# Performance work log

Measured on AMD Instinct MI355X. Metric: run time of the kernel, lower is better.

The kernel has to match this reference:

```python
import jax, jax.numpy as jnp
import numpy as np
import math

N_HEADS = 8
LN_EPS = 1e-5


def _segment_softmax(att, seg, n):
    # att: [E, H], seg: [E] target-node ids; grouped softmax over edges per target node
    m = jax.ops.segment_max(att, seg, num_segments=n)
    e = jnp.exp(att - m[seg])
    d = jax.ops.segment_sum(e, seg, num_segments=n)
    return e / (d[seg] + 1e-16)


def _layernorm(h, g, b):
    mu = jnp.mean(h, axis=-1, keepdims=True)
    var = jnp.mean((h - mu) ** 2, axis=-1, keepdims=True)
    return (h - mu) * jax.lax.rsqrt(var + LN_EPS) * g + b


def setup_inputs() -> dict:
    key = jax.random.key(0)
    ks = jax.random.split(key, 16)
    T, N, E, Din, Dh = 3, 20000, 100000, 128, 128
    s = 0.02
    x = jax.random.normal(ks[0], (T, N, Din), dtype=jnp.float32)
    edge_index = jax.random.randint(ks[1], (T, 2, E), 0, N, dtype=jnp.int64)
    return {
        "x": x,
        "edge_index": edge_index,
        "Wq": jax.random.normal(ks[2], (Din, Dh), jnp.float32) * s,
        "bq": jnp.zeros((Dh,), jnp.float32),
        "Wk": jax.random.normal(ks[3], (Din, Dh), jnp.float32) * s,
        "bk": jnp.zeros((Dh,), jnp.float32),
        "Wv": jax.random.normal(ks[4], (Din, Dh), jnp.float32) * s,
        "bv": jnp.zeros((Dh,), jnp.float32),
        "ln_g": jnp.ones((Dh,), jnp.float32),
        "ln_b": jnp.zeros((Dh,), jnp.float32),
        "W1": jax.random.normal(ks[5], (Dh, 2 * Dh), jnp.float32) * s,
        "b1": jnp.zeros((2 * Dh,), jnp.float32),
        "W2": jax.random.normal(ks[6], (2 * Dh, Dh), jnp.float32) * s,
        "b2": jnp.zeros((Dh,), jnp.float32),
    }


def reference(x, edge_index, Wq, bq, Wk, bk, Wv, bv, ln_g, ln_b, W1, b1, W2, b2):
    T, N, _ = x.shape
    Dh = Wq.shape[1]
    dk = Dh // N_HEADS
    inv_sqrt_dk = 1.0 / math.sqrt(dk)

    def ffn(h):
        r = _layernorm(h, ln_g, ln_b)
        r = jax.nn.gelu(r @ W1 + b1, approximate=False)
        r = r @ W2 + b2
        return h + r

    xs, cs, ss = [], [], []
    for t_tar in range(T):
        x_tar = x[t_tar]  # [N, Din]
        # collect edges of times 0..t_tar
        tgt = jnp.concatenate([edge_index[t, 1] for t in range(t_tar + 1)])  # [Ec]
        x_tar_e = x_tar[tgt]  # [Ec, Din]
        x_src_e = jnp.concatenate(
            [x[t][edge_index[t, 0]] for t in range(t_tar + 1)], axis=0
        )  # [Ec, Din]

        q = (x_tar_e @ Wq + bq).reshape(-1, N_HEADS, dk)
        k = (x_src_e @ Wk + bk).reshape(-1, N_HEADS, dk)
        v = (x_src_e @ Wv + bv).reshape(-1, N_HEADS, dk)
        att = jnp.sum(q * k, axis=-1) * inv_sqrt_dk  # [Ec, H]

        res_att = _segment_softmax(att, tgt, N)
        spu_att = _segment_softmax(-att, tgt, N)
        res = (v * res_att[..., None]).reshape(-1, Dh)
        spu = (v * spu_att[..., None]).reshape(-1, Dh)
        causal_hat = jax.ops.segment_sum(res, tgt, num_segments=N)
        spurious_hat = jax.ops.segment_sum(spu, tgt, num_segments=N)

        causal = ffn(causal_hat + x_tar)
        spurious = ffn(spurious_hat)
        xs.append(causal + spurious)
        cs.append(causal)
        ss.append(spurious)
    return (jnp.stack(xs), jnp.stack(cs), jnp.stack(ss))
```

## Files before the change

### kernel.cpp

```cpp
#include <hip/hip_runtime.h>
#include <hip/hip_bf16.h>

#define DEV_INLINE __device__ __forceinline__

namespace {

constexpr int T = 3;
constexpr int NN = 20000;
constexpr int NE = 100000;
constexpr int D = 128;
constexpr int D2 = 256;
constexpr int NROW = T * NN;
constexpr size_t OUTSZ = (size_t)T * NN * D;
constexpr int NTILE = T * (NN / 16);

typedef __attribute__((ext_vector_type(8))) short bf16x8;
typedef __attribute__((ext_vector_type(4))) float f32x4;
typedef __attribute__((ext_vector_type(2))) _Float16 h2;
typedef __hip_bfloat16 bf16;

DEV_INLINE unsigned short f2bf(float f) {
  __hip_bfloat16 t = __float2bfloat16(f);
  return *(unsigned short*)&t;
}

__global__ void k_detect(const unsigned int* __restrict__ ei32, int* __restrict__ flag) {
  int nz = 0;
  for (int i = threadIdx.x; i < 4096; i += 256)
    nz |= (ei32[2 * i + 1] != 0u);
  if (__any(nz) && (threadIdx.x & 63) == 0) atomicOr(&flag[0], 1);
}

DEV_INLINE int loadIdx(const void* ei, int is32, long long idx) {
  return is32 ? ((const int*)ei)[idx] : (int)((const long long*)ei)[idx];
}

__global__ void k_count(const void* __restrict__ ei, const int* __restrict__ flag,
                        int* __restrict__ counts) {
  int i = blockIdx.x * blockDim.x + threadIdx.x;
  if (i >= T * NE) return;
  int is32 = flag[0];
  int t = i / NE, e = i - t * NE;
  int tgt = loadIdx(ei, is32, (long long)(t * 2 + 1) * NE + e);
  atomicAdd(&counts[t * NN + tgt], 1);
}

__global__ void k_scan(const int* __restrict__ counts, int* __restrict__ offsets,
                       int* __restrict__ cursor) {
  int t = blockIdx.x;
  const int* c = counts + t * NN;
  int* o = offsets + t * (NN + 1);
  int* cur = cursor + t * NN;
  __shared__ int part[256];
  int tid = threadIdx.x;
  constexpr int CH = (NN + 255) / 256;
  int b = tid * CH;
  int e = min(b + CH, NN);
  int s = 0;
  for (int i = b; i < e; i++) s += c[i];
  part[tid] = s;
  __syncthreads();
  for (int d = 1; d < 256; d <<= 1) {
    int v = (tid >= d) ? part[tid - d] : 0;
    __syncthreads();
    part[tid] += v;
    __syncthreads();
  }
  int run = part[tid] - s;
  for (int i = b; i < e; i++) { o[i] = run; cur[i] = run; run += c[i]; }
  if (tid == 255) o[NN] = part[255];
}

__global__ void k_scatter(const void* __restrict__ ei, const int* __restrict__ flag,
                          int* __restrict__ cursor, int* __restrict__ elist) {
  int i = blockIdx.x * blockDim.x + threadIdx.x;
  if (i >= T * NE) return;
  int is32 = flag[0];
  int t = i / NE, e = i - t * NE;
  int src = loadIdx(ei, is32, (long long)(t * 2 + 0) * NE + e);
  int tgt = loadIdx(ei, is32, (long long)(t * 2 + 1) * NE + e);
  int pos = atomicAdd(&cursor[t * NN + tgt], 1);
  elist[t * NE + pos] = src;
}

__global__ void k_precast(const float* __restrict__ Wq, const float* __restrict__ Wk,
                          const float* __restrict__ Wv, const float* __restrict__ W1,
                          const float* __restrict__ W2, bf16* __restrict__ WqkvT,
                          bf16* __restrict__ W1L, bf16* __restrict__ W2L) {
  int i0 = blockIdx.x * blockDim.x + threadIdx.x;
  int stride = gridDim.x * blockDim.x;
  for (int j = i0; j < 384 * 128; j += stride) {
    int c = j >> 7, k = j & 127;
    float v = c < 128 ? Wq[k * D + c]
                      : (c < 256 ? Wk[k * D + (c - 128)] : Wv[k * D + (c - 256)]);
    WqkvT[c * 128 + k] = __float2bfloat16(v);
  }
  for (int idx = i0; idx < 4 * 256 * 32; idx += stride) {
    int j = idx & 31, c = (idx >> 5) & 255, kk = idx >> 13;
    W1L[idx] = __float2bfloat16(W1[(kk * 32 + j) * D2 + c]);
  }
  for (int idx = i0; idx < 8 * 128 * 32; idx += stride) {
    int j = idx & 31, c = (idx >> 5) & 127, kk = idx >> 12;
    W2L[idx] = __float2bfloat16(W2[(kk * 32 + j) * D + c]);
  }
}

__global__ __launch_bounds__(256) void k_qkv_mfma(
    const float* __restrict__ x, const bf16* __restrict__ WqkvT,
    const float* __restrict__ bq, const float* __restrict__ bk,
    const float* __restrict__ bv,
    _Float16* __restrict__ Qh, uint2* __restrict__ KV) {
  __shared__ char As[64 * 256];
  __shared__ char Bs[384 * 80];
  int row0 = blockIdx.x * 64;
  int tid = threadIdx.x;
  for (int i = tid; i < 64 * 16; i += 256) {
    int rr = i >> 4, kb = i & 15;
    int grow = row0 + rr;
    uint4 v = make_uint4(0, 0, 0, 0);
    if (grow < NROW) {
      float4 lo = *(const float4*)&x[(size_t)grow * D + kb * 8];
      float4 hi = *(const float4*)&x[(size_t)grow * D + kb * 8 + 4];
      v.x = ((unsigned)f2bf(lo.y) << 16) | f2bf(lo.x);
      v.y = ((unsigned)f2bf(lo.w) << 16) | f2bf(lo.z);
      v.z = ((unsigned)f2bf(hi.y) << 16) | f2bf(hi.x);
      v.w = ((unsigned)f2bf(hi.w) << 16) | f2bf(hi.z);
    }
    *(uint4*)(As + rr * 256 + ((kb * 16) ^ ((rr & 7) << 4))) = v;
  }
  int wid = tid >> 6, lane = tid & 63;
  int lr = lane & 15, lg = lane >> 4;
  f32x4 acc[24];
#pragma unroll
  for (int i = 0; i < 24; i++) acc[i] = (f32x4){0.f, 0.f, 0.f, 0.f};
  for (int kk = 0; kk < 4; kk++) {
    __syncthreads();
    for (int i = tid; i < 384 * 4; i += 256) {
      int c = i >> 2, ko = (i & 3) * 8;
      *(uint4*)(Bs + c * 80 + ko * 2) =
          *(const uint4*)&WqkvT[(size_t)c * 128 + kk * 32 + ko];
    }
    __syncthreads();
    int ar = wid * 16 + lr;
    bf16x8 a = *(bf16x8*)(As + ar * 256 + ((kk * 64 + lg * 16) ^ ((ar & 7) << 4)));
#pragma unroll
    for (int nt = 0; nt < 24; nt++) {
      bf16x8 b = *(bf16x8*)(Bs + (nt * 16 + lr) * 80 + lg * 16);
      acc[nt] = __builtin_amdgcn_mfma_f32_16x16x32_bf16(a, b, acc[nt], 0, 0, 0);
    }
  }
#pragma unroll
  for (int nt = 0; nt < 8; nt++) {
    int c = nt * 16 + lr;
    float bb = bq[c];
#pragma unroll
    for (int j = 0; j < 4; j++) {
      int orow = row0 + wid * 16 + lg * 4 + j;
      if (orow < NROW)
        Qh[(size_t)orow * D + c] = (_Float16)((acc[nt][j] + bb) * 0.25f);
    }
  }
#pragma unroll
  for (int nt = 0; nt < 8; nt++) {
    int c = nt * 16 + lr;
    float bbk = bk[c], bbv = bv[c];
#pragma unroll
    for (int j = 0; j < 4; j++) {
      int orow = row0 + wid * 16 + lg * 4 + j;
      unsigned ku =
          (unsigned)__builtin_bit_cast(unsigned short, (_Float16)(acc[nt + 8][j] + bbk));
      unsigned vu =
          (unsigned)__builtin_bit_cast(unsigned short, (_Float16)(acc[nt + 16][j] + bbv));
      unsigned kn = __shfl_xor(ku, 1, 64);
      unsigned vn = __shfl_xor(vu, 1, 64);
      if ((lr & 1) == 0 && orow < NROW)
        KV[(size_t)orow * 64 + (c >> 1)] = make_uint2((kn << 16) | ku, (vn << 16) | vu);
    }
  }
}

DEV_INLINE float waveReduceSum(float v) {
#pragma unroll
  for (int m = 1; m < 64; m <<= 1) v += __shfl_xor(v, m, 64);
  return v;
}

template <bool B0, bool B1, bool B2>
DEV_INLINE void edgeUpdate(h2 q0, h2 q1, h2 q2, unsigned kraw, unsigned vraw,
                           float& dr0, float& ds0, float& arx0, float& ary0,
                           float& asx0, float& asy0, float& dr1, float& ds1,
                           float& arx1, float& ary1, float& asx1, float& asy1,
                           float& dr2, float& ds2, float& arx2, float& ary2,
                           float& asx2, float& asy2) {
  h2 kh = __builtin_bit_cast(h2, kraw);
  h2 vh = __builtin_bit_cast(h2, vraw);
  float vx = (float)vh[0], vy = (float)vh[1];
  float a0 = 0.f, a1 = 0.f, a2 = 0.f;
  if (B0) a0 = __builtin_amdgcn_fdot2(q0, kh, 0.f, false);
  if (B1) a1 = __builtin_amdgcn_fdot2(q1, kh, 0.f, false);
  if (B2) a2 = __builtin_amdgcn_fdot2(q2, kh, 0.f, false);
  if (B0) a0 += __shfl_xor(a0, 1, 64);
  if (B1) a1 += __shfl_xor(a1, 1, 64);
  if (B2) a2 += __shfl_xor(a2, 1, 64);
  if (B0) a0 += __shfl_xor(a0, 2, 64);
  if (B1) a1 += __shfl_xor(a1, 2, 64);
  if (B2) a2 += __shfl_xor(a2, 2, 64);
  if (B0) a0 += __shfl_xor(a0, 4, 64);
  if (B1) a1 += __shfl_xor(a1, 4, 64);
  if (B2) a2 += __shfl_xor(a2, 4, 64);
  if (B0) {
    float e = __expf(a0), f = __expf(-a0);
    dr0 += e; arx0 += e * vx; ary0 += e * vy;
    ds0 += f; asx0 += f * vx; asy0 += f * vy;
  }
  if (B1) {
    float e = __expf(a1), f = __expf(-a1);
    dr1 += e; arx1 += e * vx; ary1 += e * vy;
    ds1 += f; asx1 += f * vx; asy1 += f * vy;
  }
  if (B2) {
    float e = __expf(a2), f = __expf(-a2);
    dr2 += e; arx2 += e * vx; ary2 += e * vy;
    ds2 += f; asx2 += f * vx; asy2 += f * vy;
  }
}

__global__ __launch_bounds__(256) void k_attn(
    const _Float16* __restrict__ Qh, const uint2* __restrict__ KV,
    const float* __restrict__ x, const int* __restrict__ offsets,
    const int* __restrict__ elist, const float* __restrict__ lng,
    const float* __restrict__ lnb, float* __restrict__ h, bf16* __restrict__ rb) {
  int n = blockIdx.x * 4 + (threadIdx.x >> 6);
  int l = threadIdx.x & 63;
  float2 g2 = *(const float2*)&lng[2 * l];
  float2 b2 = *(const float2*)&lnb[2 * l];
  h2 q0 = __builtin_bit_cast(h2, *(const unsigned*)&Qh[((size_t)0 * NN + n) * D + 2 * l]);
  h2 q1 = __builtin_bit_cast(h2, *(const unsigned*)&Qh[((size_t)1 * NN + n) * D + 2 * l]);
  h2 q2 = __builtin_bit_cast(h2, *(const unsigned*)&Qh[((size_t)2 * NN + n) * D + 2 * l]);
  float dr0 = 0.f, ds0 = 0.f, arx0 = 0.f, ary0 = 0.f, asx0 = 0.f, asy0 = 0.f;
  float dr1 = 0.f, ds1 = 0.f, arx1 = 0.f, ary1 = 0.f, asx1 = 0.f, asy1 = 0.f;
  float dr2 = 0.f, ds2 = 0.f, arx2 = 0.f, ary2 = 0.f, asx2 = 0.f, asy2 = 0.f;
#define TSEC(TT, B0, B1, B2)                                                    \
  {                                                                             \
    const int* off = offsets + TT * (NN + 1);                                   \
    int b = off[n], e = off[n + 1];                                             \
    const int* el = elist + TT * NE;                                            \
    const uint2* KVt = KV + (size_t)TT * NN * 64;                               \
    for (int i = b; i < e; i++) {                                               \
      uint2 kv = KVt[(size_t)el[i] * 64 + l];                                   \
      edgeUpdate<B0, B1, B2>(q0, q1, q2, kv.x, kv.y, dr0, ds0, arx0, ary0,      \
                             asx0, asy0, dr1, ds1, arx1, ary1, asx1, asy1,      \
                             dr2, ds2, arx2, ary2, asx2, asy2);                 \
    }                                                                           \
  }
  TSEC(0, true, true, true)
  TSEC(1, false, true, true)
  TSEC(2, false, false, true)
#undef TSEC
#define EPILOGUE(TT, DR, DS, ARX, ARY, ASX, ASY)                                 \
  {                                                                              \
    float2 xr = *(const float2*)&x[((size_t)TT * NN + n) * D + 2 * l];           \
    float ir = 1.f / (DR + 1e-16f), is = 1.f / (DS + 1e-16f);                    \
    float hcx = ARX * ir + xr.x, hcy = ARY * ir + xr.y;                          \
    float hsx = ASX * is, hsy = ASY * is;                                        \
    float mu = waveReduceSum(hcx + hcy) * (1.f / 128.f);                         \
    float dx = hcx - mu, dy = hcy - mu;                                          \
    float var = waveReduceSum(dx * dx + dy * dy) * (1.f / 128.f);                \
    float rstd = rsqrtf(var + 1e-5f);                                            \
    float rcx = dx * rstd * g2.x + b2.x, rcy = dy * rstd * g2.y + b2.y;          \
    float mu2 = waveReduceSum(hsx + hsy) * (1.f / 128.f);                        \
    float ex = hsx - mu2, ey = hsy - mu2;                                        \
    float var2 = waveReduceSum(ex * ex + ey * ey) * (1.f / 128.f);               \
    float rstd2 = rsqrtf(var2 + 1e-5f);                                          \
    float rsx = ex * rstd2 * g2.x + b2.x, rsy = ey * rstd2 * g2.y + b2.y;        \
    size_t base = (size_t)TT * 2 * NN;                                           \
    size_t iC = (base + n) * D + 2 * l;                                          \
    size_t iS = (base + NN + n) * D + 2 * l;                                     \
    *(float2*)&h[iC] = make_float2(hcx, hcy);                                    \
    *(float2*)&h[iS] = make_float2(hsx, hsy);                                    \
    *(unsigned*)&rb[iC] = ((unsigned)f2bf(rcy) << 16) | f2bf(rcx);               \
    *(unsigned*)&rb[iS] = ((unsigned)f2bf(rsy) << 16) | f2bf(rsx);               \
  }
  EPILOGUE(0, dr0, ds0, arx0, ary0, asx0, asy0)
  EPILOGUE(1, dr1, ds1, arx1, ary1, asx1, asy1)
  EPILOGUE(2, dr2, ds2, arx2, ary2, asx2, asy2)
#undef EPILOGUE
}

__global__ __launch_bounds__(512) void k_ffn_fused(
    const bf16* __restrict__ rb, const bf16* __restrict__ W1L,
    const bf16* __restrict__ W2L, const float* __restrict__ b1,
    const float* __restrict__ b2, const float* __restrict__ h,
    float* __restrict__ out) {
  __shared__ char As[32 * 256];
  __shared__ char Gs[32 * 528];
  int tid = threadIdx.x;
  int wid = tid >> 6, lane = tid & 63;
  int lr = lane & 15, lg = lane >> 4;
  int wr = (wid & 1) * 16;
  int wc1 = (wid >> 1) * 64;
  int wc2 = (wid >> 1) * 32;
  int ar = wr + lr;
  bf16x8 w1f[4][4];
#pragma unroll
  for (int kk = 0; kk < 4; kk++)
#pragma unroll
    for (int nt = 0; nt < 4; nt++)
      w1f[kk][nt] =
          *(const bf16x8*)&W1L[((size_t)kk * 256 + wc1 + nt * 16 + lr) * 32 + lg * 8];
  bf16x8 w2f[8][2];
#pragma unroll
  for (int kk = 0; kk < 8; kk++)
#pragma unroll
    for (int nt = 0; nt < 2; nt++)
      w2f[kk][nt] =
          *(const bf16x8*)&W2L[((size_t)kk * 128 + wc2 + nt * 16 + lr) * 32 + lg * 8];
  float bb1[4], bb2[2];
#pragma unroll
  for (int nt = 0; nt < 4; nt++) bb1[nt] = b1[wc1 + nt * 16 + lr];
#pragma unroll
  for (int nt = 0; nt < 2; nt++) bb2[nt] = b2[wc2 + nt * 16 + lr];
  int srr = tid >> 4, skb = tid & 15;
  int tile = blockIdx.x;
  uint4 pref;
  {
    int t2 = tile / 1250, nb = tile - t2 * 1250;
    size_t grow = (size_t)t2 * 2 * NN + (size_t)(srr >> 4) * NN + nb * 16 + (srr & 15);
    pref = *(const uint4*)&rb[grow * D + skb * 8];
  }
  for (; tile < NTILE; tile += gridDim.x) {
    int t2 = tile / 1250, nb = tile - t2 * 1250;
    int n0 = nb * 16;
    size_t base = (size_t)t2 * 2 * NN;
    *(uint4*)(As + srr * 256 + ((skb * 16) ^ ((srr & 7) << 4))) = pref;
    float hpref[2][4];
#pragma unroll
    for (int nt = 0; nt < 2; nt++) {
      int c = wc2 + nt * 16 + lr;
#pragma unroll
      for (int j = 0; j < 4; j++) {
        int rr2 = wr + lg * 4 + j;
        hpref[nt][j] = h[(base + (size_t)(rr2 >> 4) * NN + n0 + (rr2 & 15)) * D + c];
      }
    }
    int ntile = tile + gridDim.x;
    if (ntile < NTILE) {
      int t2n = ntile / 1250, nbn = ntile - t2n * 1250;
      size_t grow =
          (size_t)t2n * 2 * NN + (size_t)(srr >> 4) * NN + nbn * 16 + (srr & 15);
      pref = *(const uint4*)&rb[grow * D + skb * 8];
    }
    __syncthreads();
    f32x4 acc1[4];
#pragma unroll
    for (int i = 0; i < 4; i++) acc1[i] = (f32x4){0.f, 0.f, 0.f, 0.f};
#pragma unroll
    for (int kk = 0; kk < 4; kk++) {
      bf16x8 a = *(bf16x8*)(As + ar * 256 + ((kk * 64 + lg * 16) ^ ((ar & 7) << 4)));
#pragma unroll
      for (int nt = 0; nt < 4; nt++)
        acc1[nt] =
            __builtin_amdgcn_mfma_f32_16x16x32_bf16(a, w1f[kk][nt], acc1[nt], 0, 0, 0);
    }
#pragma unroll
    for (int nt = 0; nt < 4; nt++) {
      int c = wc1 + nt * 16 + lr;
#pragma unroll
      for (int j = 0; j < 4; j++) {
        int r = wr + lg * 4 + j;
        float y = acc1[nt][j] + bb1[nt];
        y = 0.5f * y * (1.f + erff(y * 0.70710678118654752f));
        unsigned us = f2bf(y);
        unsigned nbv = __shfl_xor(us, 1, 64);
        if ((lr & 1) == 0) *(unsigned*)(Gs + r * 528 + c * 2) = (nbv << 16) | us;
      }
    }
    __syncthreads();
    f32x4 acc2[2];
#pragma unroll
    for (int i = 0; i < 2; i++) acc2[i] = (f32x4){0.f, 0.f, 0.f, 0.f};
#pragma unroll
    for (int kk = 0; kk < 8; kk++) {
      bf16x8 a = *(bf16x8*)(Gs + ar * 528 + kk * 64 + lg * 16);
#pragma unroll
      for (int nt = 0; nt < 2; nt++)
        acc2[nt] =
            __builtin_amdgcn_mfma_f32_16x16x32_bf16(a, w2f[kk][nt], acc2[nt], 0, 0, 0);
    }
    __syncthreads();
    float* zbuf = (float*)Gs;
#pragma unroll
    for (int nt = 0; nt < 2; nt++) {
      int c = wc2 + nt * 16 + lr;
#pragma unroll
      for (int j = 0; j < 4; j++) {
        int rr2 = wr + lg * 4 + j;
        int side = rr2 >> 4;
        int node = n0 + (rr2 & 15);
        float z = acc2[nt][j] + bb2[nt] + hpref[nt][j];
        out[(size_t)(1 + side) * OUTSZ + ((size_t)t2 * NN + node) * D + c] = z;
        zbuf[rr2 * 132 + c] = z;
      }
    }
    __syncthreads();
    for (int i = tid; i < 16 * 128; i += 512) {
      int node = i >> 7, c = i & 127;
      out[((size_t)t2 * NN + n0 + node) * D + c] =
          zbuf[node * 132 + c] + zbuf[(node + 16) * 132 + c];
    }
  }
}

}

extern "C" void kernel_launch(void* const* d_in, const int* in_sizes, int n_in,
                              void* d_out, int out_size, void* d_ws, size_t ws_size,
                              hipStream_t stream) {
  const float* x = (const float*)d_in[0];
  const void* ei = d_in[1];
  const float* Wq = (const float*)d_in[2];
  const float* bq = (const float*)d_in[3];
  const float* Wk = (const float*)d_in[4];
  const float* bk = (const float*)d_in[5];
  const float* Wv = (const float*)d_in[6];
  const float* bv = (const float*)d_in[7];
  const float* lng = (const float*)d_in[8];
  const float* lnb = (const float*)d_in[9];
  const float* W1 = (const float*)d_in[10];
  const float* b1 = (const float*)d_in[11];
  const float* W2 = (const float*)d_in[12];
  const float* b2 = (const float*)d_in[13];
  float* out = (float*)d_out;

  char* ws = (char*)d_ws;
  size_t off = 0;
  auto alloc = [&](size_t bytes) -> void* {
    void* p = ws + off;
    off += (bytes + 255) & ~(size_t)255;
    return p;
  };
  bf16* WqkvT = (bf16*)alloc((size_t)384 * 128 * 2);
  bf16* W1L = (bf16*)alloc((size_t)128 * 256 * 2);
  bf16* W2L = (bf16*)alloc((size_t)256 * 128 * 2);
  _Float16* Qh = (_Float16*)alloc((size_t)NROW * D * 2);
  uint2* KV = (uint2*)alloc((size_t)NROW * 64 * 8);
  float* h = (float*)alloc((size_t)T * 2 * NN * D * 4);
  bf16* rb = (bf16*)alloc((size_t)T * 2 * NN * D * 2);
  int* counts = (int*)alloc((size_t)T * NN * 4);
  int* offsets = (int*)alloc((size_t)T * (NN + 1) * 4);
  int* cursor = (int*)alloc((size_t)T * NN * 4);
  int* elist = (int*)alloc((size_t)T * NE * 4);
  int* dflag = (int*)alloc(256);

  hipMemsetAsync(counts, 0, (size_t)T * NN * 4, stream);
  hipMemsetAsync(dflag, 0, 8, stream);
  k_detect<<<1, 256, 0, stream>>>((const unsigned int*)ei, dflag);
  int eb = (T * NE + 255) / 256;
  k_count<<<eb, 256, 0, stream>>>(ei, dflag, counts);
  k_scan<<<T, 256, 0, stream>>>(counts, offsets, cursor);
  k_scatter<<<eb, 256, 0, stream>>>(ei, dflag, cursor, elist);
  k_precast<<<128, 256, 0, stream>>>(Wq, Wk, Wv, W1, W2, WqkvT, W1L, W2L);
  k_qkv_mfma<<<(NROW + 63) / 64, 256, 0, stream>>>(x, WqkvT, bq, bk, bv, Qh, KV);
  k_attn<<<NN / 4, 256, 0, stream>>>(Qh, KV, x, offsets, elist, lng, lnb, h, rb);
  k_ffn_fused<<<512, 512, 0, stream>>>(rb, W1L, W2L, b1, b2, h, out);
}
```

Baseline: 253.6 us.

## Process two edges per wavefront in attention and store residual h as bf16

The attention kernel now splits each wavefront into two half-waves. Each half handles a different edge, with every lane covering four channels through a 16-byte KV load, and the partial sums are combined at the end with a cross-half shuffle. This halves the serial edge-loop trip count and the shuffle-reduction depth per edge, adding a masked tail for odd edge counts. Separately, the residual h buffer is stored in bf16 instead of fp32 to cut write and read traffic between the attention and FFN kernels, at some cost in residual precision.

```diff
diff --git a/kernel.cpp b/kernel.cpp
--- a/kernel.cpp
+++ b/kernel.cpp
@@ -23,6 +23,7 @@
   __hip_bfloat16 t = __float2bfloat16(f);
   return *(unsigned short*)&t;
 }
+DEV_INLINE float bf2f(unsigned short u) { return __uint_as_float((unsigned)u << 16); }
 
 __global__ void k_detect(const unsigned int* __restrict__ ei32, int* __restrict__ flag) {
   int nz = 0;
@@ -185,43 +186,28 @@
   return v;
 }
 
-template <bool B0, bool B1, bool B2>
-DEV_INLINE void edgeUpdate(h2 q0, h2 q1, h2 q2, unsigned kraw, unsigned vraw,
-                           float& dr0, float& ds0, float& arx0, float& ary0,
-                           float& asx0, float& asy0, float& dr1, float& ds1,
-                           float& arx1, float& ary1, float& asx1, float& asy1,
-                           float& dr2, float& ds2, float& arx2, float& ary2,
-                           float& asx2, float& asy2) {
-  h2 kh = __builtin_bit_cast(h2, kraw);
-  h2 vh = __builtin_bit_cast(h2, vraw);
-  float vx = (float)vh[0], vy = (float)vh[1];
-  float a0 = 0.f, a1 = 0.f, a2 = 0.f;
-  if (B0) a0 = __builtin_amdgcn_fdot2(q0, kh, 0.f, false);
-  if (B1) a1 = __builtin_amdgcn_fdot2(q1, kh, 0.f, false);
-  if (B2) a2 = __builtin_amdgcn_fdot2(q2, kh, 0.f, false);
-  if (B0) a0 += __shfl_xor(a0, 1, 64);
-  if (B1) a1 += __shfl_xor(a1, 1, 64);
-  if (B2) a2 += __shfl_xor(a2, 1, 64);
-  if (B0) a0 += __shfl_xor(a0, 2, 64);
-  if (B1) a1 += __shfl_xor(a1, 2, 64);
-  if (B2) a2 += __shfl_xor(a2, 2, 64);
-  if (B0) a0 += __shfl_xor(a0, 4, 64);
-  if (B1) a1 += __shfl_xor(a1, 4, 64);
-  if (B2) a2 += __shfl_xor(a2, 4, 64);
-  if (B0) {
-    float e = __expf(a0), f = __expf(-a0);
-    dr0 += e; arx0 += e * vx; ary0 += e * vy;
-    ds0 += f; asx0 += f * vx; asy0 += f * vy;
-  }
-  if (B1) {
-    float e = __expf(a1), f = __expf(-a1);
-    dr1 += e; arx1 += e * vx; ary1 += e * vy;
-    ds1 += f; asx1 += f * vx; asy1 += f * vy;
-  }
-  if (B2) {
-    float e = __expf(a2), f = __expf(-a2);
-    dr2 += e; arx2 += e * vx; ary2 += e * vy;
-    ds2 += f; asx2 += f * vx; asy2 += f * vy;
+template <int TS, bool TAIL>
+DEV_INLINE void procPair(uint4 kv, const h2* q01, const h2* q23, float* dr, float* ds,
+                         float (*ar)[4], float (*as)[4], float valid) {
+  h2 k01 = __builtin_bit_cast(h2, kv.x);
+  h2 v01 = __builtin_bit_cast(h2, kv.y);
+  h2 k23 = __builtin_bit_cast(h2, kv.z);
+  h2 v23 = __builtin_bit_cast(h2, kv.w);
+  float v0 = (float)v01[0], v1 = (float)v01[1];
+  float v2 = (float)v23[0], v3 = (float)v23[1];
+#pragma unroll
+  for (int tt = TS; tt < 3; tt++) {
+    float a = __builtin_amdgcn_fdot2(q23[tt], k23, 0.f, false);
+    a = __builtin_amdgcn_fdot2(q01[tt], k01, a, false);
+    a += __shfl_xor(a, 1, 64);
+    a += __shfl_xor(a, 2, 64);
+    float e = __expf(a), f = __expf(-a);
+    if (TAIL) { e *= valid; f *= valid; }
+    dr[tt] += e; ds[tt] += f;
+    ar[tt][0] += e * v0; ar[tt][1] += e * v1;
+    ar[tt][2] += e * v2; ar[tt][3] += e * v3;
+    as[tt][0] += f * v0; as[tt][1] += f * v1;
+    as[tt][2] += f * v2; as[tt][3] += f * v3;
   }
 }
 
@@ -229,68 +215,106 @@
     const _Float16* __restrict__ Qh, const uint2* __restrict__ KV,
     const float* __restrict__ x, const int* __restrict__ offsets,
     const int* __restrict__ elist, const float* __restrict__ lng,
-    const float* __restrict__ lnb, float* __restrict__ h, bf16* __restrict__ rb) {
+    const float* __restrict__ lnb, bf16* __restrict__ hB, bf16* __restrict__ rb) {
   int n = blockIdx.x * 4 + (threadIdx.x >> 6);
   int l = threadIdx.x & 63;
-  float2 g2 = *(const float2*)&lng[2 * l];
-  float2 b2 = *(const float2*)&lnb[2 * l];
-  h2 q0 = __builtin_bit_cast(h2, *(const unsigned*)&Qh[((size_t)0 * NN + n) * D + 2 * l]);
-  h2 q1 = __builtin_bit_cast(h2, *(const unsigned*)&Qh[((size_t)1 * NN + n) * D + 2 * l]);
-  h2 q2 = __builtin_bit_cast(h2, *(const unsigned*)&Qh[((size_t)2 * NN + n) * D + 2 * l]);
-  float dr0 = 0.f, ds0 = 0.f, arx0 = 0.f, ary0 = 0.f, asx0 = 0.f, asy0 = 0.f;
-  float dr1 = 0.f, ds1 = 0.f, arx1 = 0.f, ary1 = 0.f, asx1 = 0.f, asy1 = 0.f;
-  float dr2 = 0.f, ds2 = 0.f, arx2 = 0.f, ary2 = 0.f, asx2 = 0.f, asy2 = 0.f;
-#define TSEC(TT, B0, B1, B2)                                                    \
-  {                                                                             \
-    const int* off = offsets + TT * (NN + 1);                                   \
-    int b = off[n], e = off[n + 1];                                             \
-    const int* el = elist + TT * NE;                                            \
-    const uint2* KVt = KV + (size_t)TT * NN * 64;                               \
-    for (int i = b; i < e; i++) {                                               \
-      uint2 kv = KVt[(size_t)el[i] * 64 + l];                                   \
-      edgeUpdate<B0, B1, B2>(q0, q1, q2, kv.x, kv.y, dr0, ds0, arx0, ary0,      \
-                             asx0, asy0, dr1, ds1, arx1, ary1, asx1, asy1,      \
-                             dr2, ds2, arx2, ary2, asx2, asy2);                 \
-    }                                                                           \
-  }
-  TSEC(0, true, true, true)
-  TSEC(1, false, true, true)
-  TSEC(2, false, false, true)
+  int sl = l & 31, half = l >> 5;
+  h2 q01[3], q23[3];
+#pragma unroll
+  for (int tt = 0; tt < 3; tt++) {
+    uint2 qu = *(const uint2*)&Qh[((size_t)tt * NN + n) * D + 4 * sl];
+    q01[tt] = __builtin_bit_cast(h2, qu.x);
+    q23[tt] = __builtin_bit_cast(h2, qu.y);
+  }
+  float dr[3] = {0.f, 0.f, 0.f}, ds[3] = {0.f, 0.f, 0.f};
+  float ar[3][4] = {{0.f}}, as[3][4] = {{0.f}};
+#define TSEC(TT)                                                              \
+  {                                                                           \
+    const int* off = offsets + TT * (NN + 1);                                 \
+    int b = off[n], e = off[n + 1];                                           \
+    const int* el = elist + TT * NE;                                          \
+    const uint2* KVt = KV + (size_t)TT * NN * 64;                             \
+    int i = b;                                                                \
+    for (; i + 2 <= e; i += 2) {                                              \
+      int s = el[i + half];                                                   \
+      uint4 kv = *(const uint4*)&KVt[(size_t)s * 64 + 2 * sl];                \
+      procPair<TT, false>(kv, q01, q23, dr, ds, ar, as, 1.f);                 \
+    }                                                                         \
+    if (i < e) {                                                              \
+      int s = el[i];                                                          \
+      uint4 kv = *(const uint4*)&KVt[(size_t)s * 64 + 2 * sl];                \
+      procPair<TT, true>(kv, q01, q23, dr, ds, ar, as, half ? 0.f : 1.f);     \
+    }                                                                         \
+  }
+  TSEC(0)
+  TSEC(1)
+  TSEC(2)
 #undef TSEC
-#define EPILOGUE(TT, DR, DS, ARX, ARY, ASX, ASY)                                 \
-  {                                                                              \
-    float2 xr = *(const float2*)&x[((size_t)TT * NN + n) * D + 2 * l];           \
-    float ir = 1.f / (DR + 1e-16f), is = 1.f / (DS + 1e-16f);                    \
-    float hcx = ARX * ir + xr.x, hcy = ARY * ir + xr.y;                          \
-    float hsx = ASX * is, hsy = ASY * is;                                        \
-    float mu = waveReduceSum(hcx + hcy) * (1.f / 128.f);                         \
-    float dx = hcx - mu, dy = hcy - mu;                                          \
-    float var = waveReduceSum(dx * dx + dy * dy) * (1.f / 128.f);                \
-    float rstd = rsqrtf(var + 1e-5f);                                            \
-    float rcx = dx * rstd * g2.x + b2.x, rcy = dy * rstd * g2.y + b2.y;          \
-    float mu2 = waveReduceSum(hsx + hsy) * (1.f / 128.f);                        \
-    float ex = hsx - mu2, ey = hsy - mu2;                                        \
-    float var2 = waveReduceSum(ex * ex + ey * ey) * (1.f / 128.f);               \
-    float rstd2 = rsqrtf(var2 + 1e-5f);                                          \
-    float rsx = ex * rstd2 * g2.x + b2.x, rsy = ey * rstd2 * g2.y + b2.y;        \
-    size_t base = (size_t)TT * 2 * NN;                                           \
-    size_t iC = (base + n) * D + 2 * l;                                          \
-    size_t iS = (base + NN + n) * D + 2 * l;                                     \
-    *(float2*)&h[iC] = make_float2(hcx, hcy);                                    \
-    *(float2*)&h[iS] = make_float2(hsx, hsy);                                    \
-    *(unsigned*)&rb[iC] = ((unsigned)f2bf(rcy) << 16) | f2bf(rcx);               \
-    *(unsigned*)&rb[iS] = ((unsigned)f2bf(rsy) << 16) | f2bf(rsx);               \
-  }
-  EPILOGUE(0, dr0, ds0, arx0, ary0, asx0, asy0)
-  EPILOGUE(1, dr1, ds1, arx1, ary1, asx1, asy1)
-  EPILOGUE(2, dr2, ds2, arx2, ary2, asx2, asy2)
-#undef EPILOGUE
+#pragma unroll
+  for (int tt = 0; tt < 3; tt++) {
+    dr[tt] += __shfl_xor(dr[tt], 32, 64);
+    ds[tt] += __shfl_xor(ds[tt], 32, 64);
+#pragma unroll
+    for (int d4 = 0; d4 < 4; d4++) {
+      ar[tt][d4] += __shfl_xor(ar[tt][d4], 32, 64);
+      as[tt][d4] += __shfl_xor(as[tt][d4], 32, 64);
+    }
+  }
+  float4 g4 = *(const float4*)&lng[4 * sl];
+  float4 b4 = *(const float4*)&lnb[4 * sl];
+#pragma unroll
+  for (int tt = 0; tt < 3; tt++) {
+    float4 xr = *(const float4*)&x[((size_t)tt * NN + n) * D + 4 * sl];
+    float ir = 1.f / (dr[tt] + 1e-16f), is = 1.f / (ds[tt] + 1e-16f);
+    float hc[4], hs[4];
+    hc[0] = ar[tt][0] * ir + xr.x;
+    hc[1] = ar[tt][1] * ir + xr.y;
+    hc[2] = ar[tt][2] * ir + xr.z;
+    hc[3] = ar[tt][3] * ir + xr.w;
+#pragma unroll
+    for (int j = 0; j < 4; j++) hs[j] = as[tt][j] * is;
+    float mu = waveReduceSum(hc[0] + hc[1] + hc[2] + hc[3]) * (1.f / 256.f);
+    float dx[4], ss = 0.f;
+#pragma unroll
+    for (int j = 0; j < 4; j++) { dx[j] = hc[j] - mu; ss += dx[j] * dx[j]; }
+    float var = waveReduceSum(ss) * (1.f / 256.f);
+    float rstd = rsqrtf(var + 1e-5f);
+    float rc[4];
+    rc[0] = dx[0] * rstd * g4.x + b4.x;
+    rc[1] = dx[1] * rstd * g4.y + b4.y;
+    rc[2] = dx[2] * rstd * g4.z + b4.z;
+    rc[3] = dx[3] * rstd * g4.w + b4.w;
+    float mu2 = waveReduceSum(hs[0] + hs[1] + hs[2] + hs[3]) * (1.f / 256.f);
+    float ex[4], ss2 = 0.f;
+#pragma unroll
+    for (int j = 0; j < 4; j++) { ex[j] = hs[j] - mu2; ss2 += ex[j] * ex[j]; }
+    float var2 = waveReduceSum(ss2) * (1.f / 256.f);
+    float rstd2 = rsqrtf(var2 + 1e-5f);
+    float rs[4];
+    rs[0] = ex[0] * rstd2 * g4.x + b4.x;
+    rs[1] = ex[1] * rstd2 * g4.y + b4.y;
+    rs[2] = ex[2] * rstd2 * g4.z + b4.z;
+    rs[3] = ex[3] * rstd2 * g4.w + b4.w;
+    if (half == 0) {
+      size_t base = (size_t)tt * 2 * NN;
+      size_t iC = (base + n) * D + 4 * sl;
+      size_t iS = (base + NN + n) * D + 4 * sl;
+      *(uint2*)&hB[iC] = make_uint2(((unsigned)f2bf(hc[1]) << 16) | f2bf(hc[0]),
+                                    ((unsigned)f2bf(hc[3]) << 16) | f2bf(hc[2]));
+      *(uint2*)&hB[iS] = make_uint2(((unsigned)f2bf(hs[1]) << 16) | f2bf(hs[0]),
+                                    ((unsigned)f2bf(hs[3]) << 16) | f2bf(hs[2]));
+      *(uint2*)&rb[iC] = make_uint2(((unsigned)f2bf(rc[1]) << 16) | f2bf(rc[0]),
+                                    ((unsigned)f2bf(rc[3]) << 16) | f2bf(rc[2]));
+      *(uint2*)&rb[iS] = make_uint2(((unsigned)f2bf(rs[1]) << 16) | f2bf(rs[0]),
+                                    ((unsigned)f2bf(rs[3]) << 16) | f2bf(rs[2]));
+    }
+  }
 }
 
 __global__ __launch_bounds__(512) void k_ffn_fused(
     const bf16* __restrict__ rb, const bf16* __restrict__ W1L,
     const bf16* __restrict__ W2L, const float* __restrict__ b1,
-    const float* __restrict__ b2, const float* __restrict__ h,
+    const float* __restrict__ b2, const bf16* __restrict__ h,
     float* __restrict__ out) {
   __shared__ char As[32 * 256];
   __shared__ char Gs[32 * 528];
@@ -340,7 +364,8 @@
 #pragma unroll
       for (int j = 0; j < 4; j++) {
         int rr2 = wr + lg * 4 + j;
-        hpref[nt][j] = h[(base + (size_t)(rr2 >> 4) * NN + n0 + (rr2 & 15)) * D + c];
+        hpref[nt][j] = bf2f(*(const unsigned short*)&h[
+            (base + (size_t)(rr2 >> 4) * NN + n0 + (rr2 & 15)) * D + c]);
       }
     }
     int ntile = tile + gridDim.x;
@@ -444,7 +469,7 @@
   bf16* W2L = (bf16*)alloc((size_t)256 * 128 * 2);
   _Float16* Qh = (_Float16*)alloc((size_t)NROW * D * 2);
   uint2* KV = (uint2*)alloc((size_t)NROW * 64 * 8);
-  float* h = (float*)alloc((size_t)T * 2 * NN * D * 4);
+  bf16* hB = (bf16*)alloc((size_t)T * 2 * NN * D * 2);
   bf16* rb = (bf16*)alloc((size_t)T * 2 * NN * D * 2);
   int* counts = (int*)alloc((size_t)T * NN * 4);
   int* offsets = (int*)alloc((size_t)T * (NN + 1) * 4);
@@ -461,6 +486,6 @@
   k_scatter<<<eb, 256, 0, stream>>>(ei, dflag, cursor, elist);
   k_precast<<<128, 256, 0, stream>>>(Wq, Wk, Wv, W1, W2, WqkvT, W1L, W2L);
   k_qkv_mfma<<<(NROW + 63) / 64, 256, 0, stream>>>(x, WqkvT, bq, bk, bv, Qh, KV);
-  k_attn<<<NN / 4, 256, 0, stream>>>(Qh, KV, x, offsets, elist, lng, lnb, h, rb);
-  k_ffn_fused<<<512, 512, 0, stream>>>(rb, W1L, W2L, b1, b2, h, out);
-}
+  k_attn<<<NN / 4, 256, 0, stream>>>(Qh, KV, x, offsets, elist, lng, lnb, hB, rb);
+  k_ffn_fused<<<512, 512, 0, stream>>>(rb, W1L, W2L, b1, b2, hB, out);
+}
```

Measured after the change: 250.7 us. Within noise of the previous version (-1.1%).
